# Kernel optimization log

Measured on AMD Instinct MI355X. Metric: run time of the kernel, lower is better.

Reference implementation:

```python
import jax, jax.numpy as jnp
import numpy as np

DIM = 1024
N_HEADS = 16
HEAD_DIM = DIM // N_HEADS
D_FF = 4096
EPS = 1e-6


def setup_inputs() -> dict:
    key = jax.random.key(0)
    ks = jax.random.split(key, 8)
    B, S = 2, 2048
    s = 0.02
    return {
        "x": jax.random.normal(ks[0], (B, S, DIM), dtype=jnp.float32),
        "mask": jnp.ones((B, 1, S, S), dtype=bool),
        "wq": jax.random.normal(ks[1], (DIM, DIM), dtype=jnp.float32) * s,
        "wk": jax.random.normal(ks[2], (DIM, DIM), dtype=jnp.float32) * s,
        "wv": jax.random.normal(ks[3], (DIM, DIM), dtype=jnp.float32) * s,
        "wo": jax.random.normal(ks[4], (DIM, DIM), dtype=jnp.float32) * s,
        "w_up": jax.random.normal(ks[5], (DIM, D_FF), dtype=jnp.float32) * s,
        "b_up": jnp.zeros((D_FF,), dtype=jnp.float32),
        "w_down": jax.random.normal(ks[6], (D_FF, DIM), dtype=jnp.float32) * s,
        "b_down": jnp.zeros((DIM,), dtype=jnp.float32),
        "ln1_a": jnp.ones((DIM,), dtype=jnp.float32),
        "ln1_b": jnp.zeros((DIM,), dtype=jnp.float32),
        "ln2_a": jnp.ones((DIM,), dtype=jnp.float32),
        "ln2_b": jnp.zeros((DIM,), dtype=jnp.float32),
    }


def _layernorm(x, alpha, bias):
    mu = jnp.mean(x, axis=-1, keepdims=True)
    # torch .std() is unbiased (ddof=1); denominator is (std + eps)
    sig = jnp.std(x, axis=-1, keepdims=True, ddof=1)
    return alpha * (x - mu) / (sig + EPS) + bias


def _attention(h, wq, wk, wv, wo):
    B, S, _ = h.shape
    q = (h @ wq).reshape(B, S, N_HEADS, HEAD_DIM).transpose(0, 2, 1, 3)
    k = (h @ wk).reshape(B, S, N_HEADS, HEAD_DIM).transpose(0, 2, 1, 3)
    v = (h @ wv).reshape(B, S, N_HEADS, HEAD_DIM).transpose(0, 2, 1, 3)
    scores = jnp.einsum("bhqd,bhkd->bhqk", q, k) / jnp.sqrt(jnp.float32(HEAD_DIM))
    # NOTE: original's masked_fill result is discarded -> mask is a no-op
    probs = jax.nn.softmax(scores, axis=-1)
    out = jnp.einsum("bhqk,bhkd->bhqd", probs, v)
    out = out.transpose(0, 2, 1, 3).reshape(B, S, DIM)
    return out @ wo


def reference(x, mask, wq, wk, wv, wo, w_up, b_up, w_down, b_down,
              ln1_a, ln1_b, ln2_a, ln2_b):
    h = _layernorm(x, ln1_a, ln1_b)
    x = x + _attention(h, wq, wk, wv, wo)
    h = _layernorm(x, ln2_a, ln2_b)
    ff = (jax.nn.relu(h @ w_up + b_up)) @ w_down + b_down
    return x + ff
```

## Files before the change

kernel.cpp:

```cpp
#include <hip/hip_runtime.h>
#include <hip/hip_bf16.h>

typedef __bf16 bf16_t;
typedef __bf16 bf16x8 __attribute__((ext_vector_type(8)));
typedef __bf16 bf16x4 __attribute__((ext_vector_type(4)));
typedef float  f32x4  __attribute__((ext_vector_type(4)));

#define DIM   1024
#define NHEAD 16
#define HD    64
#define DFF   4096
#define SEQ   2048
#define NTOK  4096

__device__ __forceinline__ void lgkm_barrier() {
  asm volatile("s_waitcnt lgkmcnt(0)\n\ts_barrier" ::: "memory");
}

struct TP {
  const float *wq, *wk, *wv, *wo, *wup, *wdown;
  bf16_t *wqkvT, *wupT, *wdownT;
};

__global__ __launch_bounds__(256)
void transpose_all(TP tp) {
  __shared__ bf16_t tile[32][33];
  const int id = blockIdx.x;
  const float* src; bf16_t* dst; int M, N, bx, by;
  if (id < 4096) {
    const int w = id >> 10, t = id & 1023;
    src = (w == 0) ? tp.wq : (w == 1) ? tp.wk : (w == 2) ? tp.wv : tp.wo;
    dst = tp.wqkvT + (long)w * DIM * DIM;
    M = DIM; N = DIM; bx = (t & 31) * 32; by = (t >> 5) * 32;
  } else if (id < 8192) {
    const int t = id - 4096;
    src = tp.wup; dst = tp.wupT; M = DIM; N = DFF;
    bx = (t & 127) * 32; by = (t >> 7) * 32;
  } else {
    const int t = id - 8192;
    src = tp.wdown; dst = tp.wdownT; M = DFF; N = DIM;
    bx = (t & 31) * 32; by = (t >> 5) * 32;
  }
  const int tt = threadIdx.x;
  const int r = tt >> 3, c4 = (tt & 7) * 4;
  f32x4 v = *(const f32x4*)&src[(long)(by + r) * N + bx + c4];
  tile[r][c4 + 0] = (bf16_t)v[0]; tile[r][c4 + 1] = (bf16_t)v[1];
  tile[r][c4 + 2] = (bf16_t)v[2]; tile[r][c4 + 3] = (bf16_t)v[3];
  __syncthreads();
  bf16x4 w4;
  w4[0] = tile[c4 + 0][r]; w4[1] = tile[c4 + 1][r];
  w4[2] = tile[c4 + 2][r]; w4[3] = tile[c4 + 3][r];
  *(bf16x4*)&dst[(long)(bx + r) * M + by + c4] = w4;
}

__global__ __launch_bounds__(256)
void layernorm_k(const float* __restrict__ x, const float* __restrict__ a,
                 const float* __restrict__ b, bf16_t* __restrict__ out) {
  const int row = blockIdx.x;
  const int t   = threadIdx.x;
  const float* xr = x + (long)row * DIM;
  f32x4 v = *(const f32x4*)&xr[t * 4];
  float s1 = v[0] + v[1] + v[2] + v[3];
  float s2 = v[0]*v[0] + v[1]*v[1] + v[2]*v[2] + v[3]*v[3];
  #pragma unroll
  for (int off = 32; off > 0; off >>= 1) {
    s1 += __shfl_down(s1, off);
    s2 += __shfl_down(s2, off);
  }
  __shared__ float r1[4], r2[4];
  if ((t & 63) == 0) { r1[t >> 6] = s1; r2[t >> 6] = s2; }
  __syncthreads();
  s1 = r1[0] + r1[1] + r1[2] + r1[3];
  s2 = r2[0] + r2[1] + r2[2] + r2[3];
  const float mu = s1 * (1.0f / DIM);
  float var = (s2 - (float)DIM * mu * mu) * (1.0f / (DIM - 1));
  var = fmaxf(var, 0.0f);
  const float inv = 1.0f / (sqrtf(var) + 1e-6f);
  f32x4 av = *(const f32x4*)&a[t * 4];
  f32x4 bv = *(const f32x4*)&b[t * 4];
  bf16x4 o;
  o[0] = (bf16_t)(av[0] * (v[0] - mu) * inv + bv[0]);
  o[1] = (bf16_t)(av[1] * (v[1] - mu) * inv + bv[1]);
  o[2] = (bf16_t)(av[2] * (v[2] - mu) * inv + bv[2]);
  o[3] = (bf16_t)(av[3] * (v[3] - mu) * inv + bv[3]);
  *(bf16x4*)&out[(long)row * DIM + t * 4] = o;
}

__global__ __launch_bounds__(256)
void reduce_wo_ln(const float* __restrict__ x, const bf16_t* __restrict__ p0,
                  const bf16_t* __restrict__ p1, const float* __restrict__ a,
                  const float* __restrict__ b, bf16_t* __restrict__ x1b,
                  bf16_t* __restrict__ h2) {
  const int row = blockIdx.x;
  const int t   = threadIdx.x;
  const long base = (long)row * DIM + t * 4;
  f32x4 v = *(const f32x4*)&x[base];
  bf16x4 pa = *(const bf16x4*)&p0[base];
  bf16x4 pb = *(const bf16x4*)&p1[base];
  bf16x4 xo;
  xo[0] = (bf16_t)(v[0] + (float)pa[0] + (float)pb[0]);
  xo[1] = (bf16_t)(v[1] + (float)pa[1] + (float)pb[1]);
  xo[2] = (bf16_t)(v[2] + (float)pa[2] + (float)pb[2]);
  xo[3] = (bf16_t)(v[3] + (float)pa[3] + (float)pb[3]);
  *(bf16x4*)&x1b[base] = xo;
  const float w0 = (float)xo[0], w1 = (float)xo[1], w2 = (float)xo[2], w3 = (float)xo[3];
  float s1 = w0 + w1 + w2 + w3;
  float s2 = w0*w0 + w1*w1 + w2*w2 + w3*w3;
  #pragma unroll
  for (int off = 32; off > 0; off >>= 1) {
    s1 += __shfl_down(s1, off);
    s2 += __shfl_down(s2, off);
  }
  __shared__ float r1[4], r2[4];
  if ((t & 63) == 0) { r1[t >> 6] = s1; r2[t >> 6] = s2; }
  __syncthreads();
  s1 = r1[0] + r1[1] + r1[2] + r1[3];
  s2 = r2[0] + r2[1] + r2[2] + r2[3];
  const float mu = s1 * (1.0f / DIM);
  float var = (s2 - (float)DIM * mu * mu) * (1.0f / (DIM - 1));
  var = fmaxf(var, 0.0f);
  const float inv = 1.0f / (sqrtf(var) + 1e-6f);
  f32x4 av = *(const f32x4*)&a[t * 4];
  f32x4 bv = *(const f32x4*)&b[t * 4];
  bf16x4 o;
  o[0] = (bf16_t)(av[0] * (w0 - mu) * inv + bv[0]);
  o[1] = (bf16_t)(av[1] * (w1 - mu) * inv + bv[1]);
  o[2] = (bf16_t)(av[2] * (w2 - mu) * inv + bv[2]);
  o[3] = (bf16_t)(av[3] * (w3 - mu) * inv + bv[3]);
  *(bf16x4*)&h2[(long)row * DIM + t * 4] = o;
}

__global__ __launch_bounds__(256)
void combine_att(const bf16_t* __restrict__ O1, const float* __restrict__ l0,
                 const float* __restrict__ l1, bf16_t* __restrict__ O0_attn) {
  const long i = ((long)blockIdx.x * 256 + threadIdx.x) * 4;
  const int n = (int)(i & (DIM - 1));
  const long t = i >> 10;
  const int h = n >> 6;
  const long lidx = ((t >> 11) * NHEAD + h) * SEQ + (t & (SEQ - 1));
  const float inv = 1.0f / (l0[lidx] + l1[lidx]);
  bf16x4 a = *(const bf16x4*)&O0_attn[i];
  bf16x4 b = *(const bf16x4*)&O1[i];
  bf16x4 o;
  o[0] = (bf16_t)(((float)a[0] + (float)b[0]) * inv);
  o[1] = (bf16_t)(((float)a[1] + (float)b[1]) * inv);
  o[2] = (bf16_t)(((float)a[2] + (float)b[2]) * inv);
  o[3] = (bf16_t)(((float)a[3] + (float)b[3]) * inv);
  *(bf16x4*)&O0_attn[i] = o;
}

__global__ __launch_bounds__(256)
void reduce_fd(const bf16_t* __restrict__ x1b, const float* __restrict__ bias,
               const bf16_t* __restrict__ p0, const bf16_t* __restrict__ p1,
               float* __restrict__ out) {
  const long i = ((long)blockIdx.x * 256 + threadIdx.x) * 4;
  const int n = (int)(i & (DIM - 1));
  bf16x4 xv = *(const bf16x4*)&x1b[i];
  f32x4 bv = *(const f32x4*)&bias[n];
  bf16x4 a = *(const bf16x4*)&p0[i];
  bf16x4 b = *(const bf16x4*)&p1[i];
  f32x4 o;
  o[0] = (float)xv[0] + bv[0] + (float)a[0] + (float)b[0];
  o[1] = (float)xv[1] + bv[1] + (float)a[1] + (float)b[1];
  o[2] = (float)xv[2] + bv[2] + (float)a[2] + (float)b[2];
  o[3] = (float)xv[3] + bv[3] + (float)a[3] + (float)b[3];
  *(f32x4*)&out[i] = o;
}

enum { EPI_QKV = 1, EPI_BIAS_RELU = 3, EPI_PART = 6 };

#define BM 128
#define BK 32

template <int EPI, int TBN>
__global__ __launch_bounds__(256)
void gemm_bt(const bf16_t* __restrict__ A, int lda,
             const bf16_t* __restrict__ BT, int ldb,
             bf16_t* __restrict__ Cb, bf16_t* __restrict__ Cb2,
             const float* __restrict__ bias,
             int M, int N, int Ks) {
  __shared__ bf16_t sA[2][BM][BK];
  __shared__ bf16_t sB[2][TBN][BK];
  const int tid  = threadIdx.x;
  int lin = blockIdx.x + gridDim.x * (blockIdx.y + gridDim.y * blockIdx.z);
  const int by_ = lin % gridDim.y; lin /= gridDim.y;
  const int bx_ = lin % gridDim.x;
  const int bz_ = lin / gridDim.x;
  const int m0   = by_ * BM;
  const int n0   = bx_ * TBN;
  const long koff = (long)bz_ * Ks;
  const int lane = tid & 63, wave = tid >> 6;
  constexpr int MI = (TBN == 128) ? 4 : 2;
  const int wm = (TBN == 128) ? (wave >> 1) * 64 : wave * 32;
  const int wn = (TBN == 128) ? (wave & 1) * 64 : 0;
  const int fm = lane & 15, fq = lane >> 4;

  const int lr = lane >> 2, lc = (lane & 3) * 8;
  const bf16_t* gA0 = &A[(long)(m0 + wave * 32 + lr) * lda + koff + lc];
  const bf16_t* gA1 = gA0 + 16 * (long)lda;
  const int brow = (TBN == 128) ? wave * 32 : wave * 16;
  const bf16_t* gB0 = &BT[(long)(n0 + brow + lr) * ldb + koff + lc];
  const bf16_t* gB1 = gB0 + 16 * (long)ldb;

  f32x4 acc[MI][4] = {};
  bf16x8 rA0, rA1, rB0, rB1;

  rA0 = *(const bf16x8*)gA0;
  rA1 = *(const bf16x8*)gA1;
  rB0 = *(const bf16x8*)gB0;
  if constexpr (TBN == 128) rB1 = *(const bf16x8*)gB1;
  gA0 += BK; gA1 += BK; gB0 += BK; gB1 += BK;
  *(bf16x8*)&sA[0][wave * 32 + lr][lc]      = rA0;
  *(bf16x8*)&sA[0][wave * 32 + 16 + lr][lc] = rA1;
  *(bf16x8*)&sB[0][brow + lr][lc]           = rB0;
  if constexpr (TBN == 128) *(bf16x8*)&sB[0][wave * 32 + 16 + lr][lc] = rB1;
  if (BK < Ks) {
    rA0 = *(const bf16x8*)gA0;
    rA1 = *(const bf16x8*)gA1;
    rB0 = *(const bf16x8*)gB0;
    if constexpr (TBN == 128) rB1 = *(const bf16x8*)gB1;
    gA0 += BK; gA1 += BK; gB0 += BK; gB1 += BK;
  }
  __syncthreads();

  int p = 0;
  for (int k0 = 0; k0 < Ks; k0 += BK, p ^= 1) {
    if (k0 + BK < Ks) {
      *(bf16x8*)&sA[p ^ 1][wave * 32 + lr][lc]      = rA0;
      *(bf16x8*)&sA[p ^ 1][wave * 32 + 16 + lr][lc] = rA1;
      *(bf16x8*)&sB[p ^ 1][brow + lr][lc]           = rB0;
      if constexpr (TBN == 128) *(bf16x8*)&sB[p ^ 1][wave * 32 + 16 + lr][lc] = rB1;
      if (k0 + 2 * BK < Ks) {
        rA0 = *(const bf16x8*)gA0;
        rA1 = *(const bf16x8*)gA1;
        rB0 = *(const bf16x8*)gB0;
        if constexpr (TBN == 128) rB1 = *(const bf16x8*)gB1;
        gA0 += BK; gA1 += BK; gB0 += BK; gB1 += BK;
      }
    }
    bf16x8 af[MI], bfr[4];
    #pragma unroll
    for (int i = 0; i < MI; i++) af[i]  = *(const bf16x8*)&sA[p][wm + i * 16 + fm][fq * 8];
    #pragma unroll
    for (int j = 0; j < 4; j++)  bfr[j] = *(const bf16x8*)&sB[p][wn + j * 16 + fm][fq * 8];
    #pragma unroll
    for (int i = 0; i < MI; i++)
      #pragma unroll
      for (int j = 0; j < 4; j++)
        acc[i][j] = __builtin_amdgcn_mfma_f32_16x16x32_bf16(af[i], bfr[j], acc[i][j], 0, 0, 0);
    lgkm_barrier();
  }

  #pragma unroll
  for (int i = 0; i < MI; i++) {
    #pragma unroll
    for (int j = 0; j < 4; j++) {
      const int mb = m0 + wm + i * 16 + fq * 4;
      const int n  = n0 + wn + j * 16 + fm;
      #pragma unroll
      for (int r = 0; r < 4; r++) {
        const int m = mb + r;
        float vv = acc[i][j][r];
        if constexpr (EPI == EPI_QKV) {
          const int mat = n >> 10, h_ = (n >> 6) & 15, d_ = n & 63;
          const int b_ = m >> 11, s_ = m & 2047;
          if (mat == 2) {
            Cb2[((long)(b_ * NHEAD + h_) * HD + d_) * SEQ + s_] = (bf16_t)vv;
          } else {
            Cb[(long)mat * (32L * SEQ * HD) + (((long)(b_ * NHEAD + h_)) * SEQ + s_) * HD + d_] = (bf16_t)vv;
          }
        } else if constexpr (EPI == EPI_BIAS_RELU) {
          Cb[(long)m * N + n] = (bf16_t)fmaxf(vv + bias[n], 0.0f);
        } else {
          bf16_t* P = bz_ ? Cb2 : Cb;
          P[(long)m * N + n] = (bf16_t)vv;
        }
      }
    }
  }
}

#define KVT 128

__device__ __forceinline__ int swz(int grp, int slot) {
  return (grp * 64 + (slot ^ ((slot >> 3) & 7) ^ (grp & 1))) * 8;
}

__global__ __launch_bounds__(256)
void flash_attn(const bf16_t* __restrict__ q, const bf16_t* __restrict__ k,
                const bf16_t* __restrict__ vt,
                bf16_t* __restrict__ O0, bf16_t* __restrict__ O1,
                float* __restrict__ l0, float* __restrict__ l1) {
  __shared__ bf16_t sK[16 * 64 * 8];
  __shared__ bf16_t sV[16 * 64 * 8];

  const int tid  = threadIdx.x;
  const int bh   = blockIdx.x & 31, qb = blockIdx.x >> 5;
  const int b    = bh >> 4, h = bh & 15;
  const int lane = tid & 63, wave = tid >> 6;
  const int fm   = lane & 15, fq = lane >> 4;
  const int qw0  = qb * 128 + wave * 32;
  const int kvbase = blockIdx.y * (SEQ / 2);
  bf16_t* Op = blockIdx.y ? O1 : O0;
  float*  lp = blockIdx.y ? l1 : l0;

  const bf16_t* qh  = q  + (long)bh * SEQ * HD;
  const bf16_t* kh  = k  + (long)bh * SEQ * HD;
  const bf16_t* vth = vt + (long)bh * HD * SEQ;

  bf16x8 bQ[2][2];
  #pragma unroll
  for (int qt = 0; qt < 2; qt++)
    #pragma unroll
    for (int kk = 0; kk < 2; kk++) {
      bf16x8 v = *(const bf16x8*)&qh[(long)(qw0 + qt * 16 + fm) * HD + kk * 32 + fq * 8];
      #pragma unroll
      for (int e = 0; e < 8; e++) v[e] = (bf16_t)((float)v[e] * 0.18033688f);
      bQ[qt][kk] = v;
    }

  bf16x8 ones;
  #pragma unroll
  for (int e = 0; e < 8; e++) ones[e] = (bf16_t)1.0f;

  f32x4 oA[4] = {}, oB[4] = {};
  f32x4 oLA = {}, oLB = {};

  for (int it = 0; it < (SEQ / 2) / KVT; it++) {
    const int kv0 = kvbase + it * KVT;
    __syncthreads();
    #pragma unroll
    for (int p = 0; p < 4; p++) {
      const int id = tid + p * 256;
      {
        const int rho = id >> 3, c0 = (id & 7) * 8;
        const int u = rho >> 5, w = rho & 31;
        const int h2 = (w >> 2) & 1;
        const int fmw = ((w >> 3) << 2) | (w & 3);
        const int kk = (id >> 2) & 1, fq3 = id & 3;
        bf16x8 g = *(const bf16x8*)&kh[(long)(kv0 + rho) * HD + c0];
        *(bf16x8*)&sK[swz((u * 2 + h2) * 2 + kk, fq3 * 16 + fmw)] = g;
      }
      {
        const int d = id >> 4, c0 = (id & 15) * 8;
        const int u = c0 >> 5, fq3 = (c0 >> 3) & 3;
        const int jd = d >> 4, fmw = d & 15;
        bf16x8 g = *(const bf16x8*)&vth[(long)d * SEQ + kv0 + c0];
        *(bf16x8*)&sV[swz(u * 4 + jd, fq3 * 16 + fmw)] = g;
      }
    }
    __syncthreads();

    #pragma unroll
    for (int u = 0; u < 4; u++) {
      f32x4 stA[2], stB[2];
      #pragma unroll
      for (int h2 = 0; h2 < 2; h2++) {
        bf16x8 aK0 = *(const bf16x8*)&sK[swz((u * 2 + h2) * 2 + 0, lane)];
        bf16x8 aK1 = *(const bf16x8*)&sK[swz((u * 2 + h2) * 2 + 1, lane)];
        f32x4 z0 = {};
        z0 = __builtin_amdgcn_mfma_f32_16x16x32_bf16(aK0, bQ[0][0], z0, 0, 0, 0);
        stA[h2] = __builtin_amdgcn_mfma_f32_16x16x32_bf16(aK1, bQ[0][1], z0, 0, 0, 0);
        f32x4 z1 = {};
        z1 = __builtin_amdgcn_mfma_f32_16x16x32_bf16(aK0, bQ[1][0], z1, 0, 0, 0);
        stB[h2] = __builtin_amdgcn_mfma_f32_16x16x32_bf16(aK1, bQ[1][1], z1, 0, 0, 0);
      }
      bf16x8 pA, pB;
      #pragma unroll
      for (int h2 = 0; h2 < 2; h2++)
        #pragma unroll
        for (int r = 0; r < 4; r++) {
          pA[h2 * 4 + r] = (bf16_t)__builtin_amdgcn_exp2f(stA[h2][r]);
          pB[h2 * 4 + r] = (bf16_t)__builtin_amdgcn_exp2f(stB[h2][r]);
        }
      oLA = __builtin_amdgcn_mfma_f32_16x16x32_bf16(pA, ones, oLA, 0, 0, 0);
      oLB = __builtin_amdgcn_mfma_f32_16x16x32_bf16(pB, ones, oLB, 0, 0, 0);
      #pragma unroll
      for (int jd = 0; jd < 4; jd++) {
        bf16x8 bV = *(const bf16x8*)&sV[swz(u * 4 + jd, lane)];
        oA[jd] = __builtin_amdgcn_mfma_f32_16x16x32_bf16(pA, bV, oA[jd], 0, 0, 0);
        oB[jd] = __builtin_amdgcn_mfma_f32_16x16x32_bf16(pB, bV, oB[jd], 0, 0, 0);
      }
    }
  }

  if (fm == 0) {
    #pragma unroll
    for (int r = 0; r < 4; r++) {
      lp[(long)bh * SEQ + qw0 + fq * 4 + r]      = oLA[r];
      lp[(long)bh * SEQ + qw0 + 16 + fq * 4 + r] = oLB[r];
    }
  }

  #pragma unroll
  for (int r = 0; r < 4; r++) {
    const long rowA = ((long)b * SEQ + qw0 + fq * 4 + r) * DIM + h * HD;
    const long rowB = rowA + 16L * DIM;
    #pragma unroll
    for (int jd = 0; jd < 4; jd++) {
      Op[rowA + jd * 16 + fm] = (bf16_t)oA[jd][r];
      Op[rowB + jd * 16 + fm] = (bf16_t)oB[jd][r];
    }
  }
}

extern "C" void kernel_launch(void* const* d_in, const int* in_sizes, int n_in,
                              void* d_out, int out_size, void* d_ws, size_t ws_size,
                              hipStream_t stream) {
  (void)in_sizes; (void)n_in; (void)out_size; (void)ws_size;
  const float* x      = (const float*)d_in[0];
  const float* wq     = (const float*)d_in[2];
  const float* wk     = (const float*)d_in[3];
  const float* wv     = (const float*)d_in[4];
  const float* wo     = (const float*)d_in[5];
  const float* w_up   = (const float*)d_in[6];
  const float* b_up   = (const float*)d_in[7];
  const float* w_down = (const float*)d_in[8];
  const float* b_down = (const float*)d_in[9];
  const float* ln1a   = (const float*)d_in[10];
  const float* ln1b   = (const float*)d_in[11];
  const float* ln2a   = (const float*)d_in[12];
  const float* ln2b   = (const float*)d_in[13];

  char* ws = (char*)d_ws;
  const size_t MB = 1ull << 20;
  const size_t KB = 1ull << 10;
  float*  l0     = (float*)(ws);
  float*  l1     = (float*)(ws + 256 * KB);
  bf16_t* wqkvT  = (bf16_t*)(ws + 512 * KB);
  bf16_t* woT    = (bf16_t*)(ws + 512 * KB + 6 * MB);
  bf16_t* h      = (bf16_t*)(ws + 9 * MB);
  bf16_t* O0     = (bf16_t*)(ws + 9 * MB);
  bf16_t* attn   = (bf16_t*)(ws + 9 * MB);
  bf16_t* qkv    = (bf16_t*)(ws + 17 * MB);
  bf16_t* qd     = (bf16_t*)(ws + 17 * MB);
  bf16_t* kd     = (bf16_t*)(ws + 25 * MB);
  bf16_t* vtd    = (bf16_t*)(ws + 33 * MB);
  bf16_t* O1     = (bf16_t*)(ws + 41 * MB);
  bf16_t* p0_wo  = (bf16_t*)(ws + 17 * MB);
  bf16_t* p1_wo  = (bf16_t*)(ws + 25 * MB);
  bf16_t* x1b    = (bf16_t*)(ws + 41 * MB);
  bf16_t* h2     = (bf16_t*)(ws);
  bf16_t* wdownT = (bf16_t*)(ws + 49 * MB);
  bf16_t* wupT   = (bf16_t*)(ws + 57 * MB);
  bf16_t* ff1    = (bf16_t*)(ws + 9 * MB);
  bf16_t* p0_fd  = (bf16_t*)(ws);
  bf16_t* p1_fd  = (bf16_t*)(ws + 57 * MB);
  float*  outp   = (float*)d_out;

  const dim3 T(256);
  TP tp{wq, wk, wv, wo, w_up, w_down, wqkvT, wupT, wdownT};
  transpose_all<<<dim3(12288), T, 0, stream>>>(tp);

  layernorm_k<<<dim3(4096), T, 0, stream>>>(x, ln1a, ln1b, h);
  gemm_bt<EPI_QKV, 128><<<dim3(24, 32), T, 0, stream>>>(h, DIM, wqkvT, DIM, qkv, vtd,
                                                        nullptr, NTOK, 3072, DIM);
  flash_attn<<<dim3(512, 2), T, 0, stream>>>(qd, kd, vtd, O0, O1, l0, l1);
  combine_att<<<dim3(NTOK * DIM / 1024), T, 0, stream>>>(O1, l0, l1, attn);
  gemm_bt<EPI_PART, 64><<<dim3(16, 32, 2), T, 0, stream>>>(attn, DIM, woT, DIM, p0_wo, p1_wo,
                                                           nullptr, NTOK, DIM, DIM / 2);
  reduce_wo_ln<<<dim3(4096), T, 0, stream>>>(x, p0_wo, p1_wo, ln2a, ln2b, x1b, h2);
  gemm_bt<EPI_BIAS_RELU, 128><<<dim3(32, 32), T, 0, stream>>>(h2, DIM, wupT, DIM, ff1, nullptr,
                                                              b_up, NTOK, DFF, DIM);
  gemm_bt<EPI_PART, 64><<<dim3(16, 32, 2), T, 0, stream>>>(ff1, DFF, wdownT, DFF, p0_fd, p1_fd,
                                                           nullptr, NTOK, DIM, DFF / 2);
  reduce_fd<<<dim3(NTOK * DIM / 1024), T, 0, stream>>>(x1b, b_down, p0_fd, p1_fd, outp);
}
```

Before: 391.9 us.

## Load K and V fragments directly from global memory in flash attention

Removes the shared-memory staging of K and V tiles and their barriers. Each wave now loads its MFMA K and V^T fragments straight from global memory, 32 keys per step. This drops LDS traffic and __syncthreads, but the four waves in a block now each read the same K/V data through cache with no sharing. There is also no explicit prefetch, so global load latency may be exposed unless the compiler hoists the loads.

```diff
diff --git a/kernel.cpp b/kernel.cpp
--- a/kernel.cpp
+++ b/kernel.cpp
@@ -280,20 +280,11 @@
   }
 }
 
-#define KVT 128
-
-__device__ __forceinline__ int swz(int grp, int slot) {
-  return (grp * 64 + (slot ^ ((slot >> 3) & 7) ^ (grp & 1))) * 8;
-}
-
 __global__ __launch_bounds__(256)
 void flash_attn(const bf16_t* __restrict__ q, const bf16_t* __restrict__ k,
                 const bf16_t* __restrict__ vt,
                 bf16_t* __restrict__ O0, bf16_t* __restrict__ O1,
                 float* __restrict__ l0, float* __restrict__ l1) {
-  __shared__ bf16_t sK[16 * 64 * 8];
-  __shared__ bf16_t sV[16 * 64 * 8];
-
   const int tid  = threadIdx.x;
   const int bh   = blockIdx.x & 31, qb = blockIdx.x >> 5;
   const int b    = bh >> 4, h = bh & 15;
@@ -323,65 +314,57 @@
   #pragma unroll
   for (int e = 0; e < 8; e++) ones[e] = (bf16_t)1.0f;
 
+  const int rbase = ((fm >> 2) << 3) | (fm & 3);
+  const bf16_t* pK  = kh + (long)(kvbase + rbase) * HD + fq * 8;
+  const bf16_t* pV0 = vth + (long)fm * SEQ + kvbase + fq * 8;
+  const bf16_t* pV1 = pV0 + 16L * SEQ;
+  const bf16_t* pV2 = pV0 + 32L * SEQ;
+  const bf16_t* pV3 = pV0 + 48L * SEQ;
+
   f32x4 oA[4] = {}, oB[4] = {};
   f32x4 oLA = {}, oLB = {};
 
-  for (int it = 0; it < (SEQ / 2) / KVT; it++) {
-    const int kv0 = kvbase + it * KVT;
-    __syncthreads();
-    #pragma unroll
-    for (int p = 0; p < 4; p++) {
-      const int id = tid + p * 256;
-      {
-        const int rho = id >> 3, c0 = (id & 7) * 8;
-        const int u = rho >> 5, w = rho & 31;
-        const int h2 = (w >> 2) & 1;
-        const int fmw = ((w >> 3) << 2) | (w & 3);
-        const int kk = (id >> 2) & 1, fq3 = id & 3;
-        bf16x8 g = *(const bf16x8*)&kh[(long)(kv0 + rho) * HD + c0];
-        *(bf16x8*)&sK[swz((u * 2 + h2) * 2 + kk, fq3 * 16 + fmw)] = g;
-      }
-      {
-        const int d = id >> 4, c0 = (id & 15) * 8;
-        const int u = c0 >> 5, fq3 = (c0 >> 3) & 3;
-        const int jd = d >> 4, fmw = d & 15;
-        bf16x8 g = *(const bf16x8*)&vth[(long)d * SEQ + kv0 + c0];
-        *(bf16x8*)&sV[swz(u * 4 + jd, fq3 * 16 + fmw)] = g;
-      }
-    }
-    __syncthreads();
-
-    #pragma unroll
-    for (int u = 0; u < 4; u++) {
-      f32x4 stA[2], stB[2];
-      #pragma unroll
-      for (int h2 = 0; h2 < 2; h2++) {
-        bf16x8 aK0 = *(const bf16x8*)&sK[swz((u * 2 + h2) * 2 + 0, lane)];
-        bf16x8 aK1 = *(const bf16x8*)&sK[swz((u * 2 + h2) * 2 + 1, lane)];
-        f32x4 z0 = {};
-        z0 = __builtin_amdgcn_mfma_f32_16x16x32_bf16(aK0, bQ[0][0], z0, 0, 0, 0);
-        stA[h2] = __builtin_amdgcn_mfma_f32_16x16x32_bf16(aK1, bQ[0][1], z0, 0, 0, 0);
-        f32x4 z1 = {};
-        z1 = __builtin_amdgcn_mfma_f32_16x16x32_bf16(aK0, bQ[1][0], z1, 0, 0, 0);
-        stB[h2] = __builtin_amdgcn_mfma_f32_16x16x32_bf16(aK1, bQ[1][1], z1, 0, 0, 0);
-      }
-      bf16x8 pA, pB;
-      #pragma unroll
-      for (int h2 = 0; h2 < 2; h2++)
-        #pragma unroll
-        for (int r = 0; r < 4; r++) {
-          pA[h2 * 4 + r] = (bf16_t)__builtin_amdgcn_exp2f(stA[h2][r]);
-          pB[h2 * 4 + r] = (bf16_t)__builtin_amdgcn_exp2f(stB[h2][r]);
-        }
-      oLA = __builtin_amdgcn_mfma_f32_16x16x32_bf16(pA, ones, oLA, 0, 0, 0);
-      oLB = __builtin_amdgcn_mfma_f32_16x16x32_bf16(pB, ones, oLB, 0, 0, 0);
-      #pragma unroll
-      for (int jd = 0; jd < 4; jd++) {
-        bf16x8 bV = *(const bf16x8*)&sV[swz(u * 4 + jd, lane)];
-        oA[jd] = __builtin_amdgcn_mfma_f32_16x16x32_bf16(pA, bV, oA[jd], 0, 0, 0);
-        oB[jd] = __builtin_amdgcn_mfma_f32_16x16x32_bf16(pB, bV, oB[jd], 0, 0, 0);
-      }
-    }
+  for (int it = 0; it < (SEQ / 2) / 32; it++) {
+    bf16x8 aK00 = *(const bf16x8*)(pK);
+    bf16x8 aK01 = *(const bf16x8*)(pK + 32);
+    bf16x8 aK10 = *(const bf16x8*)(pK + 4 * HD);
+    bf16x8 aK11 = *(const bf16x8*)(pK + 4 * HD + 32);
+    bf16x8 bV0  = *(const bf16x8*)(pV0);
+    bf16x8 bV1  = *(const bf16x8*)(pV1);
+    bf16x8 bV2  = *(const bf16x8*)(pV2);
+    bf16x8 bV3  = *(const bf16x8*)(pV3);
+    pK += 32 * HD; pV0 += 32; pV1 += 32; pV2 += 32; pV3 += 32;
+
+    f32x4 stA0 = {}, stA1 = {}, stB0 = {}, stB1 = {};
+    stA0 = __builtin_amdgcn_mfma_f32_16x16x32_bf16(aK00, bQ[0][0], stA0, 0, 0, 0);
+    stA0 = __builtin_amdgcn_mfma_f32_16x16x32_bf16(aK01, bQ[0][1], stA0, 0, 0, 0);
+    stA1 = __builtin_amdgcn_mfma_f32_16x16x32_bf16(aK10, bQ[0][0], stA1, 0, 0, 0);
+    stA1 = __builtin_amdgcn_mfma_f32_16x16x32_bf16(aK11, bQ[0][1], stA1, 0, 0, 0);
+    stB0 = __builtin_amdgcn_mfma_f32_16x16x32_bf16(aK00, bQ[1][0], stB0, 0, 0, 0);
+    stB0 = __builtin_amdgcn_mfma_f32_16x16x32_bf16(aK01, bQ[1][1], stB0, 0, 0, 0);
+    stB1 = __builtin_amdgcn_mfma_f32_16x16x32_bf16(aK10, bQ[1][0], stB1, 0, 0, 0);
+    stB1 = __builtin_amdgcn_mfma_f32_16x16x32_bf16(aK11, bQ[1][1], stB1, 0, 0, 0);
+
+    bf16x8 pA, pB;
+    #pragma unroll
+    for (int r = 0; r < 4; r++) {
+      pA[r]     = (bf16_t)__builtin_amdgcn_exp2f(stA0[r]);
+      pA[4 + r] = (bf16_t)__builtin_amdgcn_exp2f(stA1[r]);
+      pB[r]     = (bf16_t)__builtin_amdgcn_exp2f(stB0[r]);
+      pB[4 + r] = (bf16_t)__builtin_amdgcn_exp2f(stB1[r]);
+    }
+
+    oLA = __builtin_amdgcn_mfma_f32_16x16x32_bf16(pA, ones, oLA, 0, 0, 0);
+    oLB = __builtin_amdgcn_mfma_f32_16x16x32_bf16(pB, ones, oLB, 0, 0, 0);
+
+    oA[0] = __builtin_amdgcn_mfma_f32_16x16x32_bf16(pA, bV0, oA[0], 0, 0, 0);
+    oB[0] = __builtin_amdgcn_mfma_f32_16x16x32_bf16(pB, bV0, oB[0], 0, 0, 0);
+    oA[1] = __builtin_amdgcn_mfma_f32_16x16x32_bf16(pA, bV1, oA[1], 0, 0, 0);
+    oB[1] = __builtin_amdgcn_mfma_f32_16x16x32_bf16(pB, bV1, oB[1], 0, 0, 0);
+    oA[2] = __builtin_amdgcn_mfma_f32_16x16x32_bf16(pA, bV2, oA[2], 0, 0, 0);
+    oB[2] = __builtin_amdgcn_mfma_f32_16x16x32_bf16(pB, bV2, oB[2], 0, 0, 0);
+    oA[3] = __builtin_amdgcn_mfma_f32_16x16x32_bf16(pA, bV3, oA[3], 0, 0, 0);
+    oB[3] = __builtin_amdgcn_mfma_f32_16x16x32_bf16(pB, bV3, oB[3], 0, 0, 0);
   }
 
   if (fm == 0) {
```

Result: slower. 467.4 us (+19.3%).
